# Performance work log

Hardware: AMD Instinct MI355X
Metric: run time of the kernel (lower is better)

Reference implementation:

```python
import jax, jax.numpy as jnp
import numpy as np

B, L, D, H, T = 256, 256, 768, 1024, 32  # batch, len_seq, input_size, hidden_size, output_size

def setup_inputs() -> dict:
    key = jax.random.key(0)
    ks = jax.random.split(key, 8)
    s = 0.05
    return {
        "x": jax.random.normal(ks[0], (B, L, D), jnp.float32),
        "h0": jnp.zeros((B, H), jnp.float32),
        "c0": jnp.zeros((B, H), jnp.float32),
        "W1": jax.random.normal(ks[1], (L, H), jnp.float32) * s,
        "b1": jnp.zeros((L,), jnp.float32),
        "W2": jax.random.normal(ks[2], (L, H), jnp.float32) * s,
        "b2": jnp.zeros((L,), jnp.float32),
        "W3": jax.random.normal(ks[3], (L, H), jnp.float32) * s,
        "b3": jnp.zeros((L,), jnp.float32),
        "W_ih": jax.random.normal(ks[4], (4 * H, 3 * D), jnp.float32) * s,
        "W_hh": jax.random.normal(ks[5], (4 * H, H), jnp.float32) * s,
        "b_ih": jnp.zeros((4 * H,), jnp.float32),
        "b_hh": jnp.zeros((4 * H,), jnp.float32),
        "output_size": T,
    }

def reference(x, h0, c0, W1, b1, W2, b2, W3, b3, W_ih, W_hh, b_ih, b_hh, output_size):
    def step(carry, _):
        h, c = carry
        # three attention heads over the sequence, driven by current hidden state
        a1 = jax.nn.softmax(h @ W1.T + b1, axis=1)  # [B, L]
        a2 = jax.nn.softmax(h @ W2.T + b2, axis=1)
        a3 = jax.nn.softmax(h @ W3.T + b3, axis=1)
        v1 = jnp.einsum('bl,bld->bd', a1, x)
        v2 = jnp.einsum('bl,bld->bd', a2, x)
        v3 = jnp.einsum('bl,bld->bd', a3, x)
        v = jnp.concatenate([v1, v2, v3], axis=-1)  # [B, 3D]
        # LSTMCell: gates ordered i, f, g, o (torch convention)
        gates = v @ W_ih.T + b_ih + h @ W_hh.T + b_hh
        i_g, f_g, g_g, o_g = jnp.split(gates, 4, axis=1)
        c_new = jax.nn.sigmoid(f_g) * c + jax.nn.sigmoid(i_g) * jnp.tanh(g_g)
        h_new = jax.nn.sigmoid(o_g) * jnp.tanh(c_new)
        return (h_new, c_new), h_new
    _, hs = jax.lax.scan(step, (h0, c0), None, length=output_size)  # hs: [T, B, H]
    return jnp.transpose(hs, (1, 0, 2))  # [B, T, H]
```

## Files before the change

kernel.cpp:

```cpp
#include <hip/hip_runtime.h>
#include <math.h>

constexpr int Bn = 256;
constexpr int Ln = 256;
constexpr int Dn = 768;
constexpr int Hn = 1024;
constexpr int Tn = 32;

constexpr int K_A = Hn;
constexpr int N_A = 3 * Ln;
constexpr int K_C = 3 * Dn + Hn;
constexpr int N_C = 4 * Hn;

constexpr int ZA = 4;
constexpr int ZC = 8;

typedef unsigned short u16;
typedef short bf16x8 __attribute__((ext_vector_type(8)));
typedef float f32x4 __attribute__((ext_vector_type(4)));

constexpr size_t BY_WCHI  = 0;
constexpr size_t BY_WCLO  = BY_WCHI  + (size_t)N_C * K_C * 2;
constexpr size_t BY_WAHI  = BY_WCLO  + (size_t)N_C * K_C * 2;
constexpr size_t BY_WALO  = BY_WAHI  + (size_t)N_A * K_A * 2;
constexpr size_t BY_AHI   = BY_WALO  + (size_t)N_A * K_A * 2;
constexpr size_t BY_ALO   = BY_AHI   + (size_t)Bn * K_C * 2;
constexpr size_t BY_BIASC = BY_ALO   + (size_t)Bn * K_C * 2;
constexpr size_t BY_B123  = BY_BIASC + (size_t)N_C * 4;
constexpr size_t BY_C     = BY_B123  + (size_t)N_A * 4;
constexpr size_t BY_LP    = BY_C     + (size_t)Bn * Hn * 4;
constexpr size_t BY_GP    = BY_LP    + (size_t)ZA * Bn * N_A * 4;

__device__ inline u16 f2bf(float f) {
    unsigned int u = __float_as_uint(f);
    u = (u + 0x7fff + ((u >> 16) & 1)) >> 16;
    return (u16)u;
}
__device__ inline float bf2f(u16 s) { return __uint_as_float((unsigned int)s << 16); }
__device__ inline void split2(float a, u16& hi, u16& lo) {
    hi = f2bf(a);
    lo = f2bf(a - bf2f(hi));
}


__global__ __launch_bounds__(256) void prep_wc(const float* __restrict__ W_ih,
                                               const float* __restrict__ W_hh,
                                               u16* __restrict__ Whi, u16* __restrict__ Wlo) {
    size_t id = (size_t)blockIdx.x * 256 + threadIdx.x;
    int n = (int)(id / K_C), j = (int)(id % K_C);
    float v = (j < 3 * Dn) ? W_ih[(size_t)n * (3 * Dn) + j]
                           : W_hh[(size_t)n * Hn + (j - 3 * Dn)];
    split2(v, Whi[id], Wlo[id]);
}

__global__ __launch_bounds__(256) void prep_wa(const float* __restrict__ W1,
                                               const float* __restrict__ W2,
                                               const float* __restrict__ W3,
                                               u16* __restrict__ Whi, u16* __restrict__ Wlo) {
    int id = blockIdx.x * 256 + threadIdx.x;
    int c = id >> 10, d = id & 1023;
    int k = c >> 8, l = c & 255;
    const float* Wk = (k == 0) ? W1 : ((k == 1) ? W2 : W3);
    split2(Wk[l * Hn + d], Whi[id], Wlo[id]);
}

__global__ __launch_bounds__(256) void prep_state(const float* __restrict__ h0,
                                                  const float* __restrict__ c0,
                                                  const float* __restrict__ b_ih,
                                                  const float* __restrict__ b_hh,
                                                  const float* __restrict__ b1,
                                                  const float* __restrict__ b2,
                                                  const float* __restrict__ b3,
                                                  u16* __restrict__ Ahi, u16* __restrict__ Alo,
                                                  float* __restrict__ c,
                                                  float* __restrict__ biasC,
                                                  float* __restrict__ bias123) {
    int gid = blockIdx.x * 256 + threadIdx.x;
    int b = gid >> 10, j = gid & 1023;
    split2(h0[gid], Ahi[(size_t)b * K_C + 3 * Dn + j], Alo[(size_t)b * K_C + 3 * Dn + j]);
    c[gid] = c0[gid];
    if (gid < N_C) biasC[gid] = b_ih[gid] + b_hh[gid];
    if (gid < N_A) {
        int k = gid >> 8, l = gid & 255;
        bias123[gid] = (k == 0 ? b1 : (k == 1 ? b2 : b3))[l];
    }
}

__device__ inline void gload16(const u16* g, u16* l) {
    __builtin_amdgcn_global_load_lds(
        (const __attribute__((address_space(1))) unsigned int*)g,
        (__attribute__((address_space(3))) unsigned int*)l, 16, 0, 0);
}

__global__ __launch_bounds__(256) void gemm_mfma3(const u16* __restrict__ Ahi,
                                                  const u16* __restrict__ Alo, int lda,
                                                  const u16* __restrict__ Whi,
                                                  const u16* __restrict__ Wlo, int ldw,
                                                  float* __restrict__ Cp, int ldc, int mtot,
                                                  int ksub, int nkstep) {
    __shared__ u16 sAhi[128 * 32];
    __shared__ u16 sAlo[128 * 32];
    __shared__ u16 sWhi[128 * 32];
    __shared__ u16 sWlo[128 * 32];

    const int t = threadIdx.x;
    const int w = t >> 6, lane = t & 63;
    const int bm = blockIdx.y * 128;
    const int bn = blockIdx.x * 128;
    const int k00 = blockIdx.z * ksub;
    Cp += (size_t)blockIdx.z * mtot * ldc;

    const u16* gsrc;
    u16* ldst;
    int ld, rb;
    if      (w == 0) { gsrc = Ahi; ldst = sAhi; ld = lda; rb = bm; }
    else if (w == 1) { gsrc = Alo; ldst = sAlo; ld = lda; rb = bm; }
    else if (w == 2) { gsrc = Whi; ldst = sWhi; ld = ldw; rb = bn; }
    else             { gsrc = Wlo; ldst = sWlo; ld = ldw; rb = bn; }
    const int srow = lane >> 2;
    const int scol = (lane & 3) * 8;

    const int wrow = (w >> 1) * 64;
    const int wcol = (w & 1) * 64;
    const int fr = lane & 15;
    const int kc = (lane >> 4) * 8;

    f32x4 acc[4][4] = {};

    for (int ks = 0; ks < nkstep; ++ks) {
        const int k0 = k00 + ks * 32;
#pragma unroll
        for (int i = 0; i < 8; ++i) {
            const u16* p = gsrc + (size_t)(rb + i * 16 + srow) * ld + k0 + scol;
            gload16(p, ldst + i * 512);
        }
        __syncthreads();

        bf16x8 ah[4], al[4], wh[4], wl[4];
#pragma unroll
        for (int f = 0; f < 4; ++f) {
            ah[f] = *(const bf16x8*)&sAhi[(wrow + f * 16 + fr) * 32 + kc];
            al[f] = *(const bf16x8*)&sAlo[(wrow + f * 16 + fr) * 32 + kc];
            wh[f] = *(const bf16x8*)&sWhi[(wcol + f * 16 + fr) * 32 + kc];
            wl[f] = *(const bf16x8*)&sWlo[(wcol + f * 16 + fr) * 32 + kc];
        }
#pragma unroll
        for (int i = 0; i < 4; ++i)
#pragma unroll
            for (int j = 0; j < 4; ++j)
                acc[i][j] = __builtin_amdgcn_mfma_f32_16x16x32_bf16(ah[i], wh[j], acc[i][j], 0, 0, 0);
#pragma unroll
        for (int i = 0; i < 4; ++i)
#pragma unroll
            for (int j = 0; j < 4; ++j)
                acc[i][j] = __builtin_amdgcn_mfma_f32_16x16x32_bf16(ah[i], wl[j], acc[i][j], 0, 0, 0);
#pragma unroll
        for (int i = 0; i < 4; ++i)
#pragma unroll
            for (int j = 0; j < 4; ++j)
                acc[i][j] = __builtin_amdgcn_mfma_f32_16x16x32_bf16(al[i], wh[j], acc[i][j], 0, 0, 0);
        __syncthreads();
    }

#pragma unroll
    for (int i = 0; i < 4; ++i)
#pragma unroll
        for (int j = 0; j < 4; ++j) {
#pragma unroll
            for (int r = 0; r < 4; ++r) {
                const int gm = bm + wrow + i * 16 + (lane >> 4) * 4 + r;
                const int gn = bn + wcol + j * 16 + (lane & 15);
                Cp[(size_t)gm * ldc + gn] = acc[i][j][r];
            }
        }
}

__global__ __launch_bounds__(768) void attn_kernel(const float* __restrict__ lp,
                                                   const float* __restrict__ bias123,
                                                   const float* __restrict__ x,
                                                   u16* __restrict__ Ahi,
                                                   u16* __restrict__ Alo) {
    __shared__ float sc[3 * Ln];

    const int b = blockIdx.x;
    const int t = threadIdx.x;

    {
        float v = bias123[t];
#pragma unroll
        for (int s = 0; s < ZA; ++s) v += lp[((size_t)s * Bn + b) * N_A + t];
        sc[t] = v;
    }
    __syncthreads();

    const int w = t >> 6, lane = t & 63;
    if (w < 3) {
        float vals[4];
        float m = -3.4e38f;
#pragma unroll
        for (int p = 0; p < 4; ++p) {
            vals[p] = sc[w * 256 + lane + p * 64];
            m = fmaxf(m, vals[p]);
        }
#pragma unroll
        for (int off = 32; off; off >>= 1) m = fmaxf(m, __shfl_xor(m, off));
        float ssum = 0.f;
#pragma unroll
        for (int p = 0; p < 4; ++p) {
            vals[p] = expf(vals[p] - m);
            ssum += vals[p];
        }
#pragma unroll
        for (int off = 32; off; off >>= 1) ssum += __shfl_xor(ssum, off);
        const float inv = 1.0f / ssum;
#pragma unroll
        for (int p = 0; p < 4; ++p) sc[w * 256 + lane + p * 64] = vals[p] * inv;
    }
    __syncthreads();

    float acc0 = 0.f, acc1 = 0.f, acc2 = 0.f;
    const float* xb = x + (size_t)b * Ln * Dn;
#pragma unroll 8
    for (int l = 0; l < Ln; ++l) {
        const float xv = xb[(size_t)l * Dn + t];
        acc0 += sc[l] * xv;
        acc1 += sc[256 + l] * xv;
        acc2 += sc[512 + l] * xv;
    }
    u16* ah = Ahi + (size_t)b * K_C;
    u16* al = Alo + (size_t)b * K_C;
    split2(acc0, ah[t],            al[t]);
    split2(acc1, ah[Dn + t],       al[Dn + t]);
    split2(acc2, ah[2 * Dn + t],   al[2 * Dn + t]);
}

__global__ __launch_bounds__(256) void lstm_kernel(const float* __restrict__ gp,
                                                   const float* __restrict__ biasC,
                                                   float* __restrict__ c,
                                                   u16* __restrict__ Ahi,
                                                   u16* __restrict__ Alo,
                                                   float* __restrict__ out,
                                                   int tstep) {
    const int gid = blockIdx.x * 256 + threadIdx.x;
    const int b = gid >> 10, j = gid & 1023;

    float ig = biasC[j], fg = biasC[Hn + j], gg = biasC[2 * Hn + j], og = biasC[3 * Hn + j];
#pragma unroll
    for (int s = 0; s < ZC; ++s) {
        const float* g = gp + ((size_t)s * Bn + b) * N_C;
        ig += g[j];
        fg += g[Hn + j];
        gg += g[2 * Hn + j];
        og += g[3 * Hn + j];
    }

    const float i_s = 1.f / (1.f + expf(-ig));
    const float f_s = 1.f / (1.f + expf(-fg));
    const float o_s = 1.f / (1.f + expf(-og));
    const float g_t = tanhf(gg);

    const float ci = c[gid];
    const float cn = f_s * ci + i_s * g_t;
    const float hn = o_s * tanhf(cn);

    c[gid] = cn;
    split2(hn, Ahi[(size_t)b * K_C + 3 * Dn + j], Alo[(size_t)b * K_C + 3 * Dn + j]);
    out[((size_t)b * Tn + tstep) * Hn + j] = hn;
}


extern "C" void kernel_launch(void* const* d_in, const int* in_sizes, int n_in,
                              void* d_out, int out_size, void* d_ws, size_t ws_size,
                              hipStream_t stream) {
    const float* x    = (const float*)d_in[0];
    const float* h0   = (const float*)d_in[1];
    const float* c0   = (const float*)d_in[2];
    const float* W1   = (const float*)d_in[3];
    const float* b1   = (const float*)d_in[4];
    const float* W2   = (const float*)d_in[5];
    const float* b2   = (const float*)d_in[6];
    const float* W3   = (const float*)d_in[7];
    const float* b3   = (const float*)d_in[8];
    const float* W_ih = (const float*)d_in[9];
    const float* W_hh = (const float*)d_in[10];
    const float* b_ih = (const float*)d_in[11];
    const float* b_hh = (const float*)d_in[12];
    float* out = (float*)d_out;

    char* ws = (char*)d_ws;
    u16*   WChi    = (u16*)(ws + BY_WCHI);
    u16*   WClo    = (u16*)(ws + BY_WCLO);
    u16*   WAhi    = (u16*)(ws + BY_WAHI);
    u16*   WAlo    = (u16*)(ws + BY_WALO);
    u16*   Ahi     = (u16*)(ws + BY_AHI);
    u16*   Alo     = (u16*)(ws + BY_ALO);
    float* biasC   = (float*)(ws + BY_BIASC);
    float* bias123 = (float*)(ws + BY_B123);
    float* cbuf    = (float*)(ws + BY_C);
    float* lp      = (float*)(ws + BY_LP);
    float* gp      = (float*)(ws + BY_GP);

    prep_wc<<<(int)(((size_t)N_C * K_C) / 256), 256, 0, stream>>>(W_ih, W_hh, WChi, WClo);
    prep_wa<<<(N_A * K_A) / 256, 256, 0, stream>>>(W1, W2, W3, WAhi, WAlo);
    prep_state<<<(Bn * Hn) / 256, 256, 0, stream>>>(h0, c0, b_ih, b_hh, b1, b2, b3,
                                                    Ahi, Alo, cbuf, biasC, bias123);

    for (int t = 0; t < Tn; ++t) {
        gemm_mfma3<<<dim3(N_A / 128, Bn / 128, ZA), 256, 0, stream>>>(
            Ahi + 3 * Dn, Alo + 3 * Dn, K_C, WAhi, WAlo, K_A,
            lp, N_A, Bn, K_A / ZA, (K_A / ZA) / 32);
        attn_kernel<<<Bn, 768, 0, stream>>>(lp, bias123, x, Ahi, Alo);
        gemm_mfma3<<<dim3(N_C / 128, Bn / 128, ZC), 256, 0, stream>>>(
            Ahi, Alo, K_C, WChi, WClo, K_C,
            gp, N_C, Bn, K_C / ZC, (K_C / ZC) / 32);
        lstm_kernel<<<(Bn * Hn) / 256, 256, 0, stream>>>(gp, biasC, cbuf, Ahi, Alo, out, t);
    }

    (void)in_sizes; (void)n_in; (void)out_size; (void)ws_size;
}
```

Before: 3.285 ms.

## Double-buffer GEMM LDS tiles with XOR swizzle and vectorize attention reduction

The split-bf16 MFMA GEMM now double-buffers its LDS tiles, issuing the global-to-LDS loads for the next k-step before computing the current one, and XOR-swizzles the column slots to cut LDS bank conflicts. The attention-weighted sum over x now uses float4 loads, with the sequence split across four thread groups whose partial sums are reduced through shared memory. This adds LDS footprint (64KB in the GEMM plus 36KB of padding in the attention kernel), which may lower occupancy. The global_load_lds writes may also not be fully ordered against the single barrier per step.

```diff
diff --git a/kernel.cpp b/kernel.cpp
--- a/kernel.cpp
+++ b/kernel.cpp
@@ -98,10 +98,7 @@
                                                   const u16* __restrict__ Wlo, int ldw,
                                                   float* __restrict__ Cp, int ldc, int mtot,
                                                   int ksub, int nkstep) {
-    __shared__ u16 sAhi[128 * 32];
-    __shared__ u16 sAlo[128 * 32];
-    __shared__ u16 sWhi[128 * 32];
-    __shared__ u16 sWlo[128 * 32];
+    __shared__ u16 smem[2 * 4 * 4096];
 
     const int t = threadIdx.x;
     const int w = t >> 6, lane = t & 63;
@@ -111,38 +108,48 @@
     Cp += (size_t)blockIdx.z * mtot * ldc;
 
     const u16* gsrc;
-    u16* ldst;
     int ld, rb;
-    if      (w == 0) { gsrc = Ahi; ldst = sAhi; ld = lda; rb = bm; }
-    else if (w == 1) { gsrc = Alo; ldst = sAlo; ld = lda; rb = bm; }
-    else if (w == 2) { gsrc = Whi; ldst = sWhi; ld = ldw; rb = bn; }
-    else             { gsrc = Wlo; ldst = sWlo; ld = ldw; rb = bn; }
-    const int srow = lane >> 2;
-    const int scol = (lane & 3) * 8;
+    if      (w == 0) { gsrc = Ahi; ld = lda; rb = bm; }
+    else if (w == 1) { gsrc = Alo; ld = lda; rb = bm; }
+    else if (w == 2) { gsrc = Whi; ld = ldw; rb = bn; }
+    else             { gsrc = Wlo; ld = ldw; rb = bn; }
+    const int srow  = lane >> 2;
+    const int scol8 = (((lane & 3) ^ ((lane >> 2) & 3)) * 8);
 
     const int wrow = (w >> 1) * 64;
     const int wcol = (w & 1) * 64;
     const int fr = lane & 15;
-    const int kc = (lane >> 4) * 8;
+    const int slot = ((lane >> 4) ^ (fr & 3)) * 8;
+
+    auto stage = [&](int ks, u16* dstbuf) {
+        const int k0 = k00 + ks * 32;
+        u16* dst = dstbuf + w * 4096;
+#pragma unroll
+        for (int i = 0; i < 8; ++i) {
+            const u16* p = gsrc + (size_t)(rb + i * 16 + srow) * ld + k0 + scol8;
+            gload16(p, dst + i * 512);
+        }
+    };
 
     f32x4 acc[4][4] = {};
 
+    stage(0, smem);
+    __syncthreads();
+
     for (int ks = 0; ks < nkstep; ++ks) {
-        const int k0 = k00 + ks * 32;
-#pragma unroll
-        for (int i = 0; i < 8; ++i) {
-            const u16* p = gsrc + (size_t)(rb + i * 16 + srow) * ld + k0 + scol;
-            gload16(p, ldst + i * 512);
-        }
-        __syncthreads();
+        const int cur = ks & 1;
+        u16* bufc = smem + cur * 16384;
+        if (ks + 1 < nkstep) stage(ks + 1, smem + (cur ^ 1) * 16384);
 
         bf16x8 ah[4], al[4], wh[4], wl[4];
 #pragma unroll
         for (int f = 0; f < 4; ++f) {
-            ah[f] = *(const bf16x8*)&sAhi[(wrow + f * 16 + fr) * 32 + kc];
-            al[f] = *(const bf16x8*)&sAlo[(wrow + f * 16 + fr) * 32 + kc];
-            wh[f] = *(const bf16x8*)&sWhi[(wcol + f * 16 + fr) * 32 + kc];
-            wl[f] = *(const bf16x8*)&sWlo[(wcol + f * 16 + fr) * 32 + kc];
+            const int ra = (wrow + f * 16 + fr) * 32;
+            const int rw = (wcol + f * 16 + fr) * 32;
+            ah[f] = *(const bf16x8*)&bufc[0 * 4096 + ra + slot];
+            al[f] = *(const bf16x8*)&bufc[1 * 4096 + ra + slot];
+            wh[f] = *(const bf16x8*)&bufc[2 * 4096 + rw + slot];
+            wl[f] = *(const bf16x8*)&bufc[3 * 4096 + rw + slot];
         }
 #pragma unroll
         for (int i = 0; i < 4; ++i)
@@ -159,6 +166,7 @@
 #pragma unroll
             for (int j = 0; j < 4; ++j)
                 acc[i][j] = __builtin_amdgcn_mfma_f32_16x16x32_bf16(al[i], wh[j], acc[i][j], 0, 0, 0);
+
         __syncthreads();
     }
 
@@ -181,6 +189,7 @@
                                                    u16* __restrict__ Ahi,
                                                    u16* __restrict__ Alo) {
     __shared__ float sc[3 * Ln];
+    __shared__ float pad[4][3 * Dn];
 
     const int b = blockIdx.x;
     const int t = threadIdx.x;
@@ -218,20 +227,31 @@
     }
     __syncthreads();
 
-    float acc0 = 0.f, acc1 = 0.f, acc2 = 0.f;
+    const int col4 = (t % 192) * 4;
+    const int grp  = t / 192;
+    float4 a0 = {0, 0, 0, 0}, a1 = {0, 0, 0, 0}, a2 = {0, 0, 0, 0};
     const float* xb = x + (size_t)b * Ln * Dn;
 #pragma unroll 8
-    for (int l = 0; l < Ln; ++l) {
-        const float xv = xb[(size_t)l * Dn + t];
-        acc0 += sc[l] * xv;
-        acc1 += sc[256 + l] * xv;
-        acc2 += sc[512 + l] * xv;
-    }
+    for (int l = grp; l < Ln; l += 4) {
+        const float4 xv = *reinterpret_cast<const float4*>(&xb[(size_t)l * Dn + col4]);
+        const float s0 = sc[l], s1 = sc[256 + l], s2 = sc[512 + l];
+        a0.x += s0 * xv.x; a0.y += s0 * xv.y; a0.z += s0 * xv.z; a0.w += s0 * xv.w;
+        a1.x += s1 * xv.x; a1.y += s1 * xv.y; a1.z += s1 * xv.z; a1.w += s1 * xv.w;
+        a2.x += s2 * xv.x; a2.y += s2 * xv.y; a2.z += s2 * xv.z; a2.w += s2 * xv.w;
+    }
+    *reinterpret_cast<float4*>(&pad[grp][0 * Dn + col4]) = a0;
+    *reinterpret_cast<float4*>(&pad[grp][1 * Dn + col4]) = a1;
+    *reinterpret_cast<float4*>(&pad[grp][2 * Dn + col4]) = a2;
+    __syncthreads();
+
     u16* ah = Ahi + (size_t)b * K_C;
     u16* al = Alo + (size_t)b * K_C;
-    split2(acc0, ah[t],            al[t]);
-    split2(acc1, ah[Dn + t],       al[Dn + t]);
-    split2(acc2, ah[2 * Dn + t],   al[2 * Dn + t]);
+#pragma unroll
+    for (int h = 0; h < 3; ++h) {
+        const float v = pad[0][h * Dn + t] + pad[1][h * Dn + t] +
+                        pad[2][h * Dn + t] + pad[3][h * Dn + t];
+        split2(v, ah[h * Dn + t], al[h * Dn + t]);
+    }
 }
 
 __global__ __launch_bounds__(256) void lstm_kernel(const float* __restrict__ gp,
```

Measured after the change: 2.997 ms. 8.8% less time.
